# Performance work log

Hardware: AMD Instinct MI355X
Metric: run time of the kernel (lower is better)

## Reference

```python
import jax, jax.numpy as jnp
import numpy as np

N_NODES = 100000
N_EDGES = 1250000
D = 64  # in_dim == hid_dim (same Linear reused by both SSGConv layers)


def setup_inputs() -> dict:
    key = jax.random.key(0)
    k1, k2, k3, k4 = jax.random.split(key, 4)
    x = jax.random.normal(k1, (N_NODES, D), dtype=jnp.float32)
    edge_index = jax.random.randint(k2, (2, N_EDGES), 0, N_NODES, dtype=jnp.int64)
    W1 = jax.random.normal(k3, (D, D), dtype=jnp.float32) * (1.0 / np.sqrt(D))
    b1 = jax.random.normal(k4, (D,), dtype=jnp.float32) * 0.01
    return {"x": x, "edge_index": edge_index, "W1": W1, "b1": b1}


def reference(x, edge_index, W1, b1):
    # SSGConv(nn1): sum-aggregate neighbor features over edge_index, then Linear.
    src = edge_index[0]
    dst = edge_index[1]
    n = x.shape[0]

    def ssg_conv(h):
        # gather source-node features per edge, scatter-add into destinations
        agg = jax.ops.segment_sum(h[src], dst, num_segments=n)  # [N, D]
        return agg @ W1.T + b1  # shared nn1 for both layers (faithful to source)

    hid = ssg_conv(x)
    out = ssg_conv(hid)
    return (out, hid)
```

## Files before the change

### kernel.cpp

```cpp
#include <hip/hip_runtime.h>

#define N_NODES 100000
#define N_EDGES 1250000
#define D 64

#define BSHIFT 9
#define BUCKETS 196
#define CAP 8192
#define CHUNK 4096
#define PA_BLOCKS ((N_EDGES + CHUNK - 1) / CHUNK)
#define LCAP 64

typedef long long ll;
typedef unsigned int uint;

__device__ __forceinline__ ushort f2bf(float f) {
    uint u = __float_as_uint(f);
    u += 0x7fffu + ((u >> 16) & 1u);
    return (ushort)(u >> 16);
}

__global__ void init_kernel(int* __restrict__ cursor, int* __restrict__ srt,
                            int* __restrict__ offs) {
    int t = threadIdx.x;
    if (t < BUCKETS) cursor[t] = t * CAP;
    if (t < 8) srt[N_EDGES + t] = 0;
    if (t == 0) offs[N_NODES] = N_EDGES;
}

__global__ __launch_bounds__(256) void bucketA_kernel(const int* __restrict__ src,
                                                      const int* __restrict__ dst,
                                                      int* __restrict__ cursor,
                                                      int* __restrict__ tmp) {
    __shared__ int lcnt[BUCKETS];
    __shared__ int list[BUCKETS * LCAP];
    int tid = threadIdx.x;
    for (int b = tid; b < BUCKETS; b += 256) lcnt[b] = 0;
    __syncthreads();

    int base = blockIdx.x * CHUNK;
    int nE = min(CHUNK, N_EDGES - base);
    for (int i = tid; i < nE; i += 256) {
        int e = base + i;
        int s = src[e], d = dst[e];
        int b = d >> BSHIFT;
        int p = atomicAdd(&lcnt[b], 1);
        list[b * LCAP + p] = s | ((d & 511) << 17);
    }
    __syncthreads();

    for (int b = tid; b < BUCKETS; b += 256) {
        int c = lcnt[b];
        if (c > 0) {
            int gb = atomicAdd(&cursor[b], c);
            for (int k = 0; k < c; ++k) tmp[gb + k] = list[b * LCAP + k];
        }
    }
}

__global__ void scanSmall_kernel(const int* __restrict__ cursor, int* __restrict__ bbase) {
    __shared__ int s[256];
    int tid = threadIdx.x;
    int x = (tid < BUCKETS) ? (cursor[tid] - tid * CAP) : 0;
    s[tid] = x;
    __syncthreads();
    for (int off = 1; off < 256; off <<= 1) {
        int v = (tid >= off) ? s[tid - off] : 0;
        __syncthreads();
        s[tid] += v;
        __syncthreads();
    }
    if (tid < BUCKETS) bbase[tid] = s[tid] - x;
}

__global__ __launch_bounds__(512) void bucketB_kernel(const int* __restrict__ cursor,
                                                      const int* __restrict__ bbase,
                                                      const int* __restrict__ tmp,
                                                      int* __restrict__ srt,
                                                      int* __restrict__ offs) {
    __shared__ int hist[512];
    __shared__ int s[512];
    __shared__ int cur[512];
    int b = blockIdx.x, tid = threadIdx.x;
    int cbase = b * CAP;
    int cnt = cursor[b] - cbase;
    int gbase = bbase[b];

    hist[tid] = 0;
    __syncthreads();
    for (int i = tid; i < cnt; i += 512) {
        int ln = tmp[cbase + i] >> 17;
        atomicAdd(&hist[ln], 1);
    }
    __syncthreads();

    int x = hist[tid];
    s[tid] = x;
    __syncthreads();
    for (int off = 1; off < 512; off <<= 1) {
        int v = (tid >= off) ? s[tid - off] : 0;
        __syncthreads();
        s[tid] += v;
        __syncthreads();
    }
    int excl = s[tid] - x;
    cur[tid] = excl;

    int node0 = b << BSHIFT;
    int nloc = min(512, N_NODES - node0);
    if (tid < nloc) offs[node0 + tid] = gbase + excl;
    __syncthreads();

    for (int i = tid; i < cnt; i += 512) {
        int v = tmp[cbase + i];
        int ln = v >> 17;
        int p = atomicAdd(&cur[ln], 1);
        srt[gbase + p] = v & 0x1FFFF;
    }
}

__global__ __launch_bounds__(256) void cvt_kernel(const float* __restrict__ x,
                                                  ushort* __restrict__ xb) {
    const int n4 = N_NODES * D / 4;
    int i = blockIdx.x * 256 + threadIdx.x;
    const int stride = gridDim.x * 256;
    for (; i < n4; i += stride) {
        float4 v = ((const float4*)x)[i];
        ushort4 o;
        o.x = f2bf(v.x); o.y = f2bf(v.y); o.z = f2bf(v.z); o.w = f2bf(v.w);
        ((ushort4*)xb)[i] = o;
    }
}

#define NBLK 2048
#define ACC4(P, M, AX, AY, AZ, AW)                        \
    {                                                     \
        float f0 = __uint_as_float((P).x << 16);          \
        float f1 = __uint_as_float((P).x & 0xffff0000u);  \
        float f2 = __uint_as_float((P).y << 16);          \
        float f3 = __uint_as_float((P).y & 0xffff0000u);  \
        AX = fmaf(f0, (M), AX); AY = fmaf(f1, (M), AY);   \
        AZ = fmaf(f2, (M), AZ); AW = fmaf(f3, (M), AW);   \
    }

__global__ __launch_bounds__(256) void fused_layer(const ushort* __restrict__ hb,
                                                   const int* __restrict__ offs,
                                                   const int* __restrict__ srt,
                                                   const float* __restrict__ W1,
                                                   const float* __restrict__ b1,
                                                   float* __restrict__ out,
                                                   ushort* __restrict__ outb) {
    __shared__ __align__(16) float rbA[4][64];
    __shared__ __align__(16) float rbB[4][64];
    const int tid  = threadIdx.x;
    const int lane = tid & 63;
    const int wid  = tid >> 6;
    const int g    = lane >> 4;
    const int sub  = lane & 15;
    const int gw   = blockIdx.x * 4 + wid;
    const int GW   = NBLK * 4;
    const int goff = g << 2;

    float4 Wreg[16];
    const float4* wrow = (const float4*)(W1 + lane * D);
#pragma unroll
    for (int i = 0; i < 16; ++i) Wreg[i] = wrow[i];
    const float bj = b1[lane];

    for (int p = gw; p < (N_NODES >> 1); p += GW) {
        const int nA = p << 1;
        const int2 o2 = *(const int2*)(offs + nA);
        const int begA = o2.x;
        const int endA = o2.y;
        const int endB = offs[nA + 2];
        const int emA = (endA > begA) ? endA - 1 : begA;
        const int emB = (endB > endA) ? endB - 1 : endA;

        float aAx = 0.f, aAy = 0.f, aAz = 0.f, aAw = 0.f;
        float aBx = 0.f, aBy = 0.f, aBz = 0.f, aBw = 0.f;

        int ebA = begA, ebB = endA;
        while (ebA < endA || ebB < endB) {
            const int eA = ebA + goff;
            const int eB = ebB + goff;
            const int cA0 = min(eA,     emA), cA1 = min(eA + 1, emA);
            const int cA2 = min(eA + 2, emA), cA3 = min(eA + 3, emA);
            const int cB0 = min(eB,     emB), cB1 = min(eB + 1, emB);
            const int cB2 = min(eB + 2, emB), cB3 = min(eB + 3, emB);
            const int sA0 = __builtin_nontemporal_load(srt + cA0);
            const int sA1 = __builtin_nontemporal_load(srt + cA1);
            const int sA2 = __builtin_nontemporal_load(srt + cA2);
            const int sA3 = __builtin_nontemporal_load(srt + cA3);
            const int sB0 = __builtin_nontemporal_load(srt + cB0);
            const int sB1 = __builtin_nontemporal_load(srt + cB1);
            const int sB2 = __builtin_nontemporal_load(srt + cB2);
            const int sB3 = __builtin_nontemporal_load(srt + cB3);
            const uint2 vA0 = *((const uint2*)(hb + (ll)sA0 * D) + sub);
            const uint2 vA1 = *((const uint2*)(hb + (ll)sA1 * D) + sub);
            const uint2 vA2 = *((const uint2*)(hb + (ll)sA2 * D) + sub);
            const uint2 vA3 = *((const uint2*)(hb + (ll)sA3 * D) + sub);
            const uint2 vB0 = *((const uint2*)(hb + (ll)sB0 * D) + sub);
            const uint2 vB1 = *((const uint2*)(hb + (ll)sB1 * D) + sub);
            const uint2 vB2 = *((const uint2*)(hb + (ll)sB2 * D) + sub);
            const uint2 vB3 = *((const uint2*)(hb + (ll)sB3 * D) + sub);
            const float mA0 = (eA     < endA) ? 1.f : 0.f;
            const float mA1 = (eA + 1 < endA) ? 1.f : 0.f;
            const float mA2 = (eA + 2 < endA) ? 1.f : 0.f;
            const float mA3 = (eA + 3 < endA) ? 1.f : 0.f;
            const float mB0 = (eB     < endB) ? 1.f : 0.f;
            const float mB1 = (eB + 1 < endB) ? 1.f : 0.f;
            const float mB2 = (eB + 2 < endB) ? 1.f : 0.f;
            const float mB3 = (eB + 3 < endB) ? 1.f : 0.f;
            ACC4(vA0, mA0, aAx, aAy, aAz, aAw);
            ACC4(vA1, mA1, aAx, aAy, aAz, aAw);
            ACC4(vA2, mA2, aAx, aAy, aAz, aAw);
            ACC4(vA3, mA3, aAx, aAy, aAz, aAw);
            ACC4(vB0, mB0, aBx, aBy, aBz, aBw);
            ACC4(vB1, mB1, aBx, aBy, aBz, aBw);
            ACC4(vB2, mB2, aBx, aBy, aBz, aBw);
            ACC4(vB3, mB3, aBx, aBy, aBz, aBw);
            ebA += 16; ebB += 16;
        }

        aAx += __shfl_xor(aAx, 16); aAy += __shfl_xor(aAy, 16);
        aAz += __shfl_xor(aAz, 16); aAw += __shfl_xor(aAw, 16);
        aBx += __shfl_xor(aBx, 16); aBy += __shfl_xor(aBy, 16);
        aBz += __shfl_xor(aBz, 16); aBw += __shfl_xor(aBw, 16);
        aAx += __shfl_xor(aAx, 32); aAy += __shfl_xor(aAy, 32);
        aAz += __shfl_xor(aAz, 32); aAw += __shfl_xor(aAw, 32);
        aBx += __shfl_xor(aBx, 32); aBy += __shfl_xor(aBy, 32);
        aBz += __shfl_xor(aBz, 32); aBw += __shfl_xor(aBw, 32);

        if (g == 0) {
            float4 t; t.x = aAx; t.y = aAy; t.z = aAz; t.w = aAw;
            *((float4*)rbA[wid] + sub) = t;
        }
        if (g == 1) {
            float4 t; t.x = aBx; t.y = aBy; t.z = aBz; t.w = aBw;
            *((float4*)rbB[wid] + sub) = t;
        }

        float oA = bj, oB = bj;
        const float4* ra = (const float4*)rbA[wid];
        const float4* rb = (const float4*)rbB[wid];
#pragma unroll
        for (int k4 = 0; k4 < 16; ++k4) {
            float4 rA = ra[k4];
            float4 rB = rb[k4];
            oA += rA.x * Wreg[k4].x + rA.y * Wreg[k4].y
                + rA.z * Wreg[k4].z + rA.w * Wreg[k4].w;
            oB += rB.x * Wreg[k4].x + rB.y * Wreg[k4].y
                + rB.z * Wreg[k4].z + rB.w * Wreg[k4].w;
        }
        __builtin_nontemporal_store(oA, out + (ll)nA * D + lane);
        __builtin_nontemporal_store(oB, out + (ll)(nA + 1) * D + lane);
        if (outb) {
            outb[(ll)nA * D + lane]       = f2bf(oA);
            outb[(ll)(nA + 1) * D + lane] = f2bf(oB);
        }
    }
}

extern "C" void kernel_launch(void* const* d_in, const int* in_sizes, int n_in,
                              void* d_out, int out_size, void* d_ws, size_t ws_size,
                              hipStream_t stream) {
    const float* x  = (const float*)d_in[0];
    const int* edge = (const int*)d_in[1];
    const float* W1 = (const float*)d_in[2];
    const float* b1 = (const float*)d_in[3];

    const int* src = edge;
    const int* dst = edge + N_EDGES;

    float* out = (float*)d_out;
    float* hid = (float*)d_out + (ll)N_NODES * D;

    ushort* xb = (ushort*)d_out;

    char* ws = (char*)d_ws;
    int* cursor   = (int*)ws;  ws += 1024;
    int* bbase    = (int*)ws;  ws += 1024;
    int* offs     = (int*)ws;  ws += ((size_t)(N_NODES + 1) * 4 + 255) & ~255ull;
    int* srt      = (int*)ws;  ws += ((size_t)(N_EDGES + 8) * 4 + 255) & ~255ull;
    ushort* hidb  = (ushort*)ws; ws += (size_t)N_NODES * D * 2;
    int* tmp      = (int*)ws;

    init_kernel<<<1, 256, 0, stream>>>(cursor, srt, offs);
    bucketA_kernel<<<PA_BLOCKS, 256, 0, stream>>>(src, dst, cursor, tmp);
    scanSmall_kernel<<<1, 256, 0, stream>>>(cursor, bbase);
    bucketB_kernel<<<BUCKETS, 512, 0, stream>>>(cursor, bbase, tmp, srt, offs);

    cvt_kernel<<<2048, 256, 0, stream>>>(x, xb);

    fused_layer<<<NBLK, 256, 0, stream>>>(xb, offs, srt, W1, b1, hid, hidb);
    fused_layer<<<NBLK, 256, 0, stream>>>(hidb, offs, srt, W1, b1, out, (ushort*)nullptr);
}
```

Before: 248.6 us.

## Fold bucket scan into bucketB, parallelize bucket flush, drop W registers for occupancy

Removes the separate single-block scan kernel by recomputing the bucket prefix scan inside every bucketB block. bucketA moves to 512 threads and flushes its per-bucket lists with one wavefront per bucket instead of one serial thread per bucket. The fused layer now reads W1 from memory inside the matvec instead of keeping 16 float4 values in registers, and adds a launch bound of 8 blocks, both aimed at higher occupancy for the latency-bound gather. It also switches the srt index loads from nontemporal to ordinary loads and templates the bf16 output branch. The trade-off is repeated W1 loads per node pair and a redundant scan in each bucketB block.

```diff
diff --git a/kernel.cpp b/kernel.cpp
--- a/kernel.cpp
+++ b/kernel.cpp
@@ -28,19 +28,20 @@
     if (t == 0) offs[N_NODES] = N_EDGES;
 }
 
-__global__ __launch_bounds__(256) void bucketA_kernel(const int* __restrict__ src,
+__global__ __launch_bounds__(512) void bucketA_kernel(const int* __restrict__ src,
                                                       const int* __restrict__ dst,
                                                       int* __restrict__ cursor,
                                                       int* __restrict__ tmp) {
     __shared__ int lcnt[BUCKETS];
+    __shared__ int gbs[BUCKETS];
     __shared__ int list[BUCKETS * LCAP];
     int tid = threadIdx.x;
-    for (int b = tid; b < BUCKETS; b += 256) lcnt[b] = 0;
+    if (tid < BUCKETS) lcnt[tid] = 0;
     __syncthreads();
 
     int base = blockIdx.x * CHUNK;
     int nE = min(CHUNK, N_EDGES - base);
-    for (int i = tid; i < nE; i += 256) {
+    for (int i = tid; i < nE; i += 512) {
         int e = base + i;
         int s = src[e], d = dst[e];
         int b = d >> BSHIFT;
@@ -49,32 +50,17 @@
     }
     __syncthreads();
 
-    for (int b = tid; b < BUCKETS; b += 256) {
+    if (tid < BUCKETS) gbs[tid] = atomicAdd(&cursor[tid], lcnt[tid]);
+    __syncthreads();
+
+    int wv = tid >> 6, lane = tid & 63;
+    for (int b = wv; b < BUCKETS; b += 8) {
         int c = lcnt[b];
-        if (c > 0) {
-            int gb = atomicAdd(&cursor[b], c);
-            for (int k = 0; k < c; ++k) tmp[gb + k] = list[b * LCAP + k];
-        }
-    }
-}
-
-__global__ void scanSmall_kernel(const int* __restrict__ cursor, int* __restrict__ bbase) {
-    __shared__ int s[256];
-    int tid = threadIdx.x;
-    int x = (tid < BUCKETS) ? (cursor[tid] - tid * CAP) : 0;
-    s[tid] = x;
-    __syncthreads();
-    for (int off = 1; off < 256; off <<= 1) {
-        int v = (tid >= off) ? s[tid - off] : 0;
-        __syncthreads();
-        s[tid] += v;
-        __syncthreads();
-    }
-    if (tid < BUCKETS) bbase[tid] = s[tid] - x;
+        if (lane < c) tmp[gbs[b] + lane] = list[b * LCAP + lane];
+    }
 }
 
 __global__ __launch_bounds__(512) void bucketB_kernel(const int* __restrict__ cursor,
-                                                      const int* __restrict__ bbase,
                                                       const int* __restrict__ tmp,
                                                       int* __restrict__ srt,
                                                       int* __restrict__ offs) {
@@ -84,7 +70,17 @@
     int b = blockIdx.x, tid = threadIdx.x;
     int cbase = b * CAP;
     int cnt = cursor[b] - cbase;
-    int gbase = bbase[b];
+
+    if (tid < 256) s[tid] = (tid < BUCKETS) ? (cursor[tid] - tid * CAP) : 0;
+    __syncthreads();
+    for (int off = 1; off < 256; off <<= 1) {
+        int v = (tid >= off && tid < 256) ? s[tid - off] : 0;
+        __syncthreads();
+        if (tid < 256) s[tid] += v;
+        __syncthreads();
+    }
+    const int gbase = s[b] - cnt;
+    __syncthreads();
 
     hist[tid] = 0;
     __syncthreads();
@@ -143,13 +139,14 @@
         AZ = fmaf(f2, (M), AZ); AW = fmaf(f3, (M), AW);   \
     }
 
-__global__ __launch_bounds__(256) void fused_layer(const ushort* __restrict__ hb,
-                                                   const int* __restrict__ offs,
-                                                   const int* __restrict__ srt,
-                                                   const float* __restrict__ W1,
-                                                   const float* __restrict__ b1,
-                                                   float* __restrict__ out,
-                                                   ushort* __restrict__ outb) {
+template<int EMIT>
+__global__ __launch_bounds__(256, 8) void fused_layer(const ushort* __restrict__ hb,
+                                                      const int* __restrict__ offs,
+                                                      const int* __restrict__ srt,
+                                                      const float* __restrict__ W1,
+                                                      const float* __restrict__ b1,
+                                                      float* __restrict__ out,
+                                                      ushort* __restrict__ outb) {
     __shared__ __align__(16) float rbA[4][64];
     __shared__ __align__(16) float rbB[4][64];
     const int tid  = threadIdx.x;
@@ -161,10 +158,7 @@
     const int GW   = NBLK * 4;
     const int goff = g << 2;
 
-    float4 Wreg[16];
     const float4* wrow = (const float4*)(W1 + lane * D);
-#pragma unroll
-    for (int i = 0; i < 16; ++i) Wreg[i] = wrow[i];
     const float bj = b1[lane];
 
     for (int p = gw; p < (N_NODES >> 1); p += GW) {
@@ -187,14 +181,14 @@
             const int cA2 = min(eA + 2, emA), cA3 = min(eA + 3, emA);
             const int cB0 = min(eB,     emB), cB1 = min(eB + 1, emB);
             const int cB2 = min(eB + 2, emB), cB3 = min(eB + 3, emB);
-            const int sA0 = __builtin_nontemporal_load(srt + cA0);
-            const int sA1 = __builtin_nontemporal_load(srt + cA1);
-            const int sA2 = __builtin_nontemporal_load(srt + cA2);
-            const int sA3 = __builtin_nontemporal_load(srt + cA3);
-            const int sB0 = __builtin_nontemporal_load(srt + cB0);
-            const int sB1 = __builtin_nontemporal_load(srt + cB1);
-            const int sB2 = __builtin_nontemporal_load(srt + cB2);
-            const int sB3 = __builtin_nontemporal_load(srt + cB3);
+            const int sA0 = srt[cA0];
+            const int sA1 = srt[cA1];
+            const int sA2 = srt[cA2];
+            const int sA3 = srt[cA3];
+            const int sB0 = srt[cB0];
+            const int sB1 = srt[cB1];
+            const int sB2 = srt[cB2];
+            const int sB3 = srt[cB3];
             const uint2 vA0 = *((const uint2*)(hb + (ll)sA0 * D) + sub);
             const uint2 vA1 = *((const uint2*)(hb + (ll)sA1 * D) + sub);
             const uint2 vA2 = *((const uint2*)(hb + (ll)sA2 * D) + sub);
@@ -245,16 +239,15 @@
         const float4* rb = (const float4*)rbB[wid];
 #pragma unroll
         for (int k4 = 0; k4 < 16; ++k4) {
-            float4 rA = ra[k4];
-            float4 rB = rb[k4];
-            oA += rA.x * Wreg[k4].x + rA.y * Wreg[k4].y
-                + rA.z * Wreg[k4].z + rA.w * Wreg[k4].w;
-            oB += rB.x * Wreg[k4].x + rB.y * Wreg[k4].y
-                + rB.z * Wreg[k4].z + rB.w * Wreg[k4].w;
+            const float4 w = wrow[k4];
+            const float4 rA = ra[k4];
+            const float4 rB = rb[k4];
+            oA += rA.x * w.x + rA.y * w.y + rA.z * w.z + rA.w * w.w;
+            oB += rB.x * w.x + rB.y * w.y + rB.z * w.z + rB.w * w.w;
         }
         __builtin_nontemporal_store(oA, out + (ll)nA * D + lane);
         __builtin_nontemporal_store(oB, out + (ll)(nA + 1) * D + lane);
-        if (outb) {
+        if (EMIT) {
             outb[(ll)nA * D + lane]       = f2bf(oA);
             outb[(ll)(nA + 1) * D + lane] = f2bf(oB);
         }
@@ -279,19 +272,17 @@
 
     char* ws = (char*)d_ws;
     int* cursor   = (int*)ws;  ws += 1024;
-    int* bbase    = (int*)ws;  ws += 1024;
     int* offs     = (int*)ws;  ws += ((size_t)(N_NODES + 1) * 4 + 255) & ~255ull;
     int* srt      = (int*)ws;  ws += ((size_t)(N_EDGES + 8) * 4 + 255) & ~255ull;
     ushort* hidb  = (ushort*)ws; ws += (size_t)N_NODES * D * 2;
     int* tmp      = (int*)ws;
 
     init_kernel<<<1, 256, 0, stream>>>(cursor, srt, offs);
-    bucketA_kernel<<<PA_BLOCKS, 256, 0, stream>>>(src, dst, cursor, tmp);
-    scanSmall_kernel<<<1, 256, 0, stream>>>(cursor, bbase);
-    bucketB_kernel<<<BUCKETS, 512, 0, stream>>>(cursor, bbase, tmp, srt, offs);
+    bucketA_kernel<<<PA_BLOCKS, 512, 0, stream>>>(src, dst, cursor, tmp);
+    bucketB_kernel<<<BUCKETS, 512, 0, stream>>>(cursor, tmp, srt, offs);
 
     cvt_kernel<<<2048, 256, 0, stream>>>(x, xb);
 
-    fused_layer<<<NBLK, 256, 0, stream>>>(xb, offs, srt, W1, b1, hid, hidb);
-    fused_layer<<<NBLK, 256, 0, stream>>>(hidb, offs, srt, W1, b1, out, (ushort*)nullptr);
-}
+    fused_layer<1><<<NBLK, 256, 0, stream>>>(xb, offs, srt, W1, b1, hid, hidb);
+    fused_layer<0><<<NBLK, 256, 0, stream>>>(hidb, offs, srt, W1, b1, out, (ushort*)nullptr);
+}
```

Result: slower. 442.5 us (+78.0%).
